# Kernel tuning notes

Measured on AMD Instinct MI355X. Metric: run time of the kernel, lower is better.

Reference implementation:

```python
import jax, jax.numpy as jnp
import numpy as np

H = 128  # hidden size
I = 256  # input size

def setup_inputs() -> dict:
    key = jax.random.key(0)
    ks = jax.random.split(key, 12)
    s_ih = 1.0 / np.sqrt(H)
    inp = {
        "x": jax.random.normal(ks[0], (256, 512, I), dtype=jnp.float32),
        # PyTorch LSTM params, gate order (i, f, g, o)
        "W_ih": jax.random.uniform(ks[1], (4 * H, I), jnp.float32, -s_ih, s_ih),
        "W_hh": jax.random.uniform(ks[2], (4 * H, H), jnp.float32, -s_ih, s_ih),
        "b_ih": jax.random.uniform(ks[3], (4 * H,), jnp.float32, -s_ih, s_ih),
        "b_hh": jax.random.uniform(ks[4], (4 * H,), jnp.float32, -s_ih, s_ih),
        "W1": jax.random.uniform(ks[5], (64, H), jnp.float32, -1/np.sqrt(H), 1/np.sqrt(H)),
        "b1": jax.random.uniform(ks[6], (64,), jnp.float32, -1/np.sqrt(H), 1/np.sqrt(H)),
        "W2": jax.random.uniform(ks[7], (32, 64), jnp.float32, -1/np.sqrt(64), 1/np.sqrt(64)),
        "b2": jax.random.uniform(ks[8], (32,), jnp.float32, -1/np.sqrt(64), 1/np.sqrt(64)),
        "W3": jax.random.uniform(ks[9], (4, 32), jnp.float32, -1/np.sqrt(32), 1/np.sqrt(32)),
        "b3": jax.random.uniform(ks[10], (4,), jnp.float32, -1/np.sqrt(32), 1/np.sqrt(32)),
    }
    return inp

def _lstm_last_hidden(x, W_ih, W_hh, b_ih, b_hh):
    B = x.shape[0]
    # Precompute input contribution for all timesteps: [B, T, 4H]
    gx = jnp.einsum("bti,gi->btg", x, W_ih) + (b_ih + b_hh)
    gx = jnp.swapaxes(gx, 0, 1)  # [T, B, 4H] for scan over time

    def step(carry, g_x):
        h, c = carry
        gates = g_x + h @ W_hh.T  # [B, 4H]
        i, f, g, o = jnp.split(gates, 4, axis=-1)
        i = jax.nn.sigmoid(i)
        f = jax.nn.sigmoid(f)
        g = jnp.tanh(g)
        o = jax.nn.sigmoid(o)
        c = f * c + i * g
        h = o * jnp.tanh(c)
        return (h, c), None

    h0 = jnp.zeros((B, H), x.dtype)
    (h, _), _ = jax.lax.scan(step, (h0, h0), gx)
    return h  # last-timestep hidden state [B, H]

def reference(x, W_ih, W_hh, b_ih, b_hh, W1, b1, W2, b2, W3, b3):
    h = _lstm_last_hidden(x, W_ih, W_hh, b_ih, b_hh)
    h = jax.nn.relu(h @ W1.T + b1)
    h = jax.nn.relu(h @ W2.T + b2)
    return h @ W3.T + b3  # [B, 4]
```

## Files before the change

### kernel.cpp

```cpp
#include <hip/hip_runtime.h>
#include <hip/hip_bf16.h>


#define TC       64
#define NCHUNK   8
#define BATCH    256
#define TSEQ     512
#define ISZ      256
#define HSZ      128
#define RB       4
#define NBLK     (BATCH / RB)
#define NGB      (2 * TC * 4)
#define HROW     144
#define GX_PER_T 131072
#define GXCH     ((size_t)TC * GX_PER_T)
#define STRT     32768
#define PF       4

#define XN       (BATCH * TSEQ * ISZ)
#define WIHN     (4 * HSZ * ISZ)
#define WHHN     (4 * HSZ * HSZ)
#define CVT_UNITS ((XN + WIHN + WHHN) / 8)

typedef __attribute__((ext_vector_type(8))) short short8;
typedef __attribute__((ext_vector_type(4))) float f32x4;

__device__ __forceinline__ void barrier_nodrain() {
    __asm__ __volatile__("s_waitcnt lgkmcnt(0)\n\ts_barrier" ::: "memory");
}

__device__ __forceinline__ float fast_rcp(float x) {
    return __builtin_amdgcn_rcpf(x);
}
__device__ __forceinline__ float sigmoidf_(float x) {
    return fast_rcp(1.0f + __expf(-x));
}
__device__ __forceinline__ float tanhf_(float x) {
    float e = __expf(2.0f * x);
    return 1.0f - 2.0f * fast_rcp(e + 1.0f);
}
__device__ __forceinline__ unsigned short f2bf(float x) {
    union { float f; unsigned u; } v; v.f = x;
    unsigned r = v.u + 0x7fffu + ((v.u >> 16) & 1u);
    return (unsigned short)(r >> 16);
}
__device__ __forceinline__ float bf2f(unsigned short b) {
    union { unsigned u; float f; } v;
    v.u = ((unsigned)b) << 16;
    return v.f;
}
__device__ __forceinline__ unsigned packbf(float lo, float hi) {
    __hip_bfloat162 h2 = __float22bfloat162_rn(make_float2(lo, hi));
    union { __hip_bfloat162 h; unsigned u; } v; v.h = h2;
    return v.u;
}
__device__ __forceinline__ float sel4(f32x4 v, int r) {
    float s01 = (r & 1) ? v[1] : v[0];
    float s23 = (r & 1) ? v[3] : v[2];
    return (r & 2) ? s23 : s01;
}

__global__ __launch_bounds__(256) void conv_kernel(
    const float* __restrict__ x, const float* __restrict__ Wih,
    const float* __restrict__ Whh,
    unsigned short* __restrict__ xb, unsigned short* __restrict__ wihb,
    unsigned short* __restrict__ whhb)
{
    const size_t stride = (size_t)gridDim.x * 256;
    for (size_t u = (size_t)blockIdx.x * 256 + threadIdx.x; u < (size_t)CVT_UNITS;
         u += stride) {
        const size_t e0 = u * 8;
        const float* s; unsigned short* d;
        if (e0 < (size_t)XN)               { s = x + e0;                 d = xb + e0; }
        else if (e0 < (size_t)(XN + WIHN)) { s = Wih + (e0 - XN);        d = wihb + (e0 - XN); }
        else                               { s = Whh + (e0 - XN - WIHN); d = whhb + (e0 - XN - WIHN); }
        float4 f0 = *(const float4*)(s);
        float4 f1 = *(const float4*)(s + 4);
        *(uint4*)(d) = (uint4){packbf(f0.x, f0.y), packbf(f0.z, f0.w),
                               packbf(f1.x, f1.y), packbf(f1.z, f1.w)};
    }
}

__global__ __launch_bounds__(512, 2) void fused_kernel(
    const unsigned short* __restrict__ xb, const unsigned short* __restrict__ wihb,
    const unsigned short* __restrict__ whhb,
    const float* __restrict__ bih, const float* __restrict__ bhh,
    const unsigned short* __restrict__ gxl, unsigned short* __restrict__ gxg,
    float* __restrict__ hc, int t0, int first, int run_lstm, int run_gemm)
{
    __shared__ __align__(16) char smem[32768];
    const int tid  = threadIdx.x;
    const int w    = tid >> 6;
    const int lane = tid & 63;
    const int n    = lane & 15;
    const int quad = lane >> 4;

    if (blockIdx.x >= NBLK) {
        if (!run_gemm) return;
        short* As = (short*)smem;
        short* Bs = (short*)(smem + 16384);

        const int gb = (int)blockIdx.x - NBLK;
        const int nt = gb & 3;
        const int mt = gb >> 2;
        const int tl = mt >> 1;
        const int b0 = (mt & 1) * 128;
        const int n0 = nt * 128;

        const int mq = w & 1;
        const int nq = w >> 1;

        const int srow = tid >> 2;
        const int skh  = (tid & 3) * 8;

        const unsigned short* xr = xb + ((size_t)(b0 + srow) * TSEQ + (size_t)(t0 + tl)) * ISZ + skh;
        const unsigned short* wr = wihb + (size_t)(n0 + srow) * ISZ + skh;

        f32x4 acc[4][2];
#pragma unroll
        for (int mi = 0; mi < 4; ++mi)
#pragma unroll
            for (int ni = 0; ni < 2; ++ni)
                acc[mi][ni] = (f32x4){0.f, 0.f, 0.f, 0.f};

        *(short8*)(&As[srow * 32 + skh]) = *(const short8*)(xr);
        *(short8*)(&Bs[srow * 32 + skh]) = *(const short8*)(wr);
        barrier_nodrain();

        for (int ks = 0; ks < 8; ++ks) {
            const int cur = (ks & 1) * 4096;
            const int nxt = 4096 - cur;
            short8 va, vb;
            if (ks < 7) {
                va = *(const short8*)(xr + (ks + 1) * 32);
                vb = *(const short8*)(wr + (ks + 1) * 32);
            }
            short8 af[4], bfr[2];
#pragma unroll
            for (int mi = 0; mi < 4; ++mi)
                af[mi] = *(const short8*)(&As[cur + (mq * 64 + mi * 16 + n) * 32 + quad * 8]);
#pragma unroll
            for (int ni = 0; ni < 2; ++ni)
                bfr[ni] = *(const short8*)(&Bs[cur + (nq * 32 + ni * 16 + n) * 32 + quad * 8]);
#pragma unroll
            for (int mi = 0; mi < 4; ++mi)
#pragma unroll
                for (int ni = 0; ni < 2; ++ni)
                    acc[mi][ni] = __builtin_amdgcn_mfma_f32_16x16x32_bf16(
                        af[mi], bfr[ni], acc[mi][ni], 0, 0, 0);
            if (ks < 7) {
                *(short8*)(&As[nxt + srow * 32 + skh]) = va;
                *(short8*)(&Bs[nxt + srow * 32 + skh]) = vb;
            }
            barrier_nodrain();
        }

#pragma unroll
        for (int ni = 0; ni < 2; ++ni) {
            const int j    = nq * 32 + ni * 16 + n;
            const int gate = n0 + j;
            const float bias = bih[gate] + bhh[gate];
            const int wj = nq * 2 + ni;
#pragma unroll
            for (int mi = 0; mi < 4; ++mi) {
                const int bb   = b0 + mq * 64 + mi * 16 + quad * 4;
                const int blk2 = bb >> 2;
                const size_t idx = ((((size_t)nt * TC + tl) * 64 + blk2) * 512) +
                                   (size_t)wj * 64 + (size_t)n * 4;
                const unsigned lo = packbf(acc[mi][ni][0] + bias, acc[mi][ni][1] + bias);
                const unsigned hi = packbf(acc[mi][ni][2] + bias, acc[mi][ni][3] + bias);
                *(uint2*)(&gxg[idx]) = (uint2){lo, hi};
            }
        }
        return;
    }

    if (!run_lstm) return;
    __builtin_amdgcn_s_setprio(1);
    short* h_lds = (short*)smem;

    const int blk  = (int)blockIdx.x;
    const int b0   = blk * RB;
    const int nb   = lane & 3;
    const int jl   = lane >> 2;
    const int j    = 16 * w + jl;
    const int rsel = jl & 3;

    short8 Af[4][4];
#pragma unroll
    for (int g = 0; g < 4; ++g) {
        const unsigned short* rowb = whhb + (size_t)(128 * g + 16 * w + n) * HSZ + 8 * quad;
#pragma unroll
        for (int ks = 0; ks < 4; ++ks)
            Af[g][ks] = *(const short8*)(rowb + 32 * ks);
    }

    float c1 = 0.f, hl1 = 0.f;
    {
        unsigned short h0 = 0;
        if (!first) {
            c1 = hc[(size_t)BATCH * HSZ + (size_t)(b0 + nb) * HSZ + j];
            h0 = f2bf(hc[(size_t)(b0 + nb) * HSZ + j]);
        }
        *(unsigned short*)&h_lds[nb * HROW + j] = h0;
    }

    const unsigned short* gp[4];
#pragma unroll
    for (int g = 0; g < 4; ++g)
        gp[g] = gxl + (((size_t)g * TC) * 64 + blk) * 512 + (size_t)w * 64 + lane;

    unsigned short gq[PF][4];
#pragma unroll
    for (int d = 0; d < PF; ++d)
#pragma unroll
        for (int g = 0; g < 4; ++g)
            gq[d][g] = gp[g][(size_t)d * STRT];

    barrier_nodrain();

    for (int t = 0; t < TC; t += PF) {
#pragma unroll
        for (int u = 0; u < PF; ++u) {
            const int tt = t + u;
            const short* hb_r = h_lds + (u & 1) * (RB * HROW);
            short*       hb_w = h_lds + ((u & 1) ^ 1) * (RB * HROW);

            short8 Bf[4];
#pragma unroll
            for (int ks = 0; ks < 4; ++ks)
                Bf[ks] = *(const short8*)(&hb_r[nb * HROW + 32 * ks + 8 * quad]);

            f32x4 acc[4];
#pragma unroll
            for (int g = 0; g < 4; ++g)
                acc[g] = __builtin_amdgcn_mfma_f32_16x16x32_bf16(
                    Af[g][0], Bf[0], (f32x4){0.f, 0.f, 0.f, 0.f}, 0, 0, 0);
#pragma unroll
            for (int ks = 1; ks < 4; ++ks)
#pragma unroll
                for (int g = 0; g < 4; ++g)
                    acc[g] = __builtin_amdgcn_mfma_f32_16x16x32_bf16(
                        Af[g][ks], Bf[ks], acc[g], 0, 0, 0);

            const float s0 = sel4(acc[0], rsel) + bf2f(gq[u][0]);
            const float s1 = sel4(acc[1], rsel) + bf2f(gq[u][1]);
            const float s2 = sel4(acc[2], rsel) + bf2f(gq[u][2]);
            const float s3 = sel4(acc[3], rsel) + bf2f(gq[u][3]);

            const int tf = (tt + PF < TC) ? (tt + PF) : (TC - 1);
#pragma unroll
            for (int g = 0; g < 4; ++g)
                gq[u][g] = gp[g][(size_t)tf * STRT];

            const float ig = sigmoidf_(s0);
            const float fg = sigmoidf_(s1);
            const float gg = tanhf_(s2);
            const float og = sigmoidf_(s3);
            c1  = fg * c1 + ig * gg;
            hl1 = og * tanhf_(c1);

            *(unsigned short*)&hb_w[nb * HROW + j] = f2bf(hl1);
            barrier_nodrain();
        }
    }

    hc[(size_t)(b0 + nb) * HSZ + j] = hl1;
    hc[(size_t)BATCH * HSZ + (size_t)(b0 + nb) * HSZ + j] = c1;
}

__global__ __launch_bounds__(64) void head_kernel(
    const float* __restrict__ hc,
    const float* __restrict__ W1, const float* __restrict__ b1,
    const float* __restrict__ W2, const float* __restrict__ b2,
    const float* __restrict__ W3, const float* __restrict__ b3,
    float* __restrict__ out)
{
    __shared__ float hs[HSZ];
    __shared__ float o1[64];
    __shared__ float o2[32];
    const int bidx = blockIdx.x;
    const int t = threadIdx.x;
    hs[t]      = hc[bidx * HSZ + t];
    hs[t + 64] = hc[bidx * HSZ + t + 64];
    __syncthreads();
    {
        float a = b1[t];
#pragma unroll 8
        for (int k = 0; k < HSZ; ++k) a += W1[t * HSZ + k] * hs[k];
        o1[t] = fmaxf(a, 0.0f);
    }
    __syncthreads();
    if (t < 32) {
        float a = b2[t];
#pragma unroll 8
        for (int k = 0; k < 64; ++k) a += W2[t * 64 + k] * o1[k];
        o2[t] = fmaxf(a, 0.0f);
    }
    __syncthreads();
    if (t < 4) {
        float a = b3[t];
#pragma unroll
        for (int k = 0; k < 32; ++k) a += W3[t * 32 + k] * o2[k];
        out[bidx * 4 + t] = a;
    }
}

extern "C" void kernel_launch(void* const* d_in, const int* in_sizes, int n_in,
                              void* d_out, int out_size, void* d_ws, size_t ws_size,
                              hipStream_t stream) {
    const float* x   = (const float*)d_in[0];
    const float* Wih = (const float*)d_in[1];
    const float* Whh = (const float*)d_in[2];
    const float* bih = (const float*)d_in[3];
    const float* bhh = (const float*)d_in[4];
    const float* W1  = (const float*)d_in[5];
    const float* b1  = (const float*)d_in[6];
    const float* W2  = (const float*)d_in[7];
    const float* b2  = (const float*)d_in[8];
    const float* W3  = (const float*)d_in[9];
    const float* b3  = (const float*)d_in[10];
    float* out = (float*)d_out;

    const size_t GXB = GXCH * sizeof(unsigned short);
    unsigned short* gx0 = (unsigned short*)d_ws;
    unsigned short* gx1 = (unsigned short*)((char*)d_ws + GXB);
    float* hc = (float*)((char*)d_ws + 2 * GXB);
    unsigned short* xb   = (unsigned short*)((char*)d_ws + 2 * GXB + 262144);
    unsigned short* wihb = xb + (size_t)XN;
    unsigned short* whhb = wihb + WIHN;

    conv_kernel<<<dim3(2048), 256, 0, stream>>>(x, Wih, Whh, xb, wihb, whhb);

    for (int k = 0; k <= NCHUNK; ++k) {
        const int run_gemm = (k < NCHUNK);
        const int run_lstm = (k > 0);
        unsigned short* gg = (k & 1) ? gx1 : gx0;
        const unsigned short* gl = ((k - 1) & 1) ? gx1 : gx0;
        fused_kernel<<<dim3(NBLK + NGB), 512, 0, stream>>>(
            xb, wihb, whhb, bih, bhh, gl, gg, hc,
            k * TC, (k == 1) ? 1 : 0, run_lstm, run_gemm);
    }

    head_kernel<<<dim3(BATCH), 64, 0, stream>>>(hc, W1, b1, W2, b2, W3, b3, out);
}
```

Measured before the change: 560.5 us.

## Interleave two batch groups per LSTM block to overlap MFMA with gate math

Each LSTM block now processes 8 batch rows as two groups of 4 whose recurrence steps are staggered. While the h·W_hh MFMAs for one group issue, the sigmoid/tanh gate math and h write for the other group run, hiding the serial latency of each timestep. This halves the number of LSTM blocks, leaving more CUs for the concurrent input-projection GEMM blocks. The occupancy hint is raised from 2 to 4 waves per EU. The added register state and extra phases per step may raise register pressure or lengthen the critical path if the overlap does not materialize.

```diff
diff --git a/kernel.cpp b/kernel.cpp
--- a/kernel.cpp
+++ b/kernel.cpp
@@ -8,14 +8,12 @@
 #define TSEQ     512
 #define ISZ      256
 #define HSZ      128
-#define RB       4
-#define NBLK     (BATCH / RB)
+#define NLB      32
 #define NGB      (2 * TC * 4)
 #define HROW     144
 #define GX_PER_T 131072
 #define GXCH     ((size_t)TC * GX_PER_T)
 #define STRT     32768
-#define PF       4
 
 #define XN       (BATCH * TSEQ * ISZ)
 #define WIHN     (4 * HSZ * ISZ)
@@ -28,7 +26,6 @@
 __device__ __forceinline__ void barrier_nodrain() {
     __asm__ __volatile__("s_waitcnt lgkmcnt(0)\n\ts_barrier" ::: "memory");
 }
-
 __device__ __forceinline__ float fast_rcp(float x) {
     return __builtin_amdgcn_rcpf(x);
 }
@@ -81,7 +78,7 @@
     }
 }
 
-__global__ __launch_bounds__(512, 2) void fused_kernel(
+__global__ __launch_bounds__(512, 4) void fused_kernel(
     const unsigned short* __restrict__ xb, const unsigned short* __restrict__ wihb,
     const unsigned short* __restrict__ whhb,
     const float* __restrict__ bih, const float* __restrict__ bhh,
@@ -95,12 +92,12 @@
     const int n    = lane & 15;
     const int quad = lane >> 4;
 
-    if (blockIdx.x >= NBLK) {
+    if (blockIdx.x >= NLB) {
         if (!run_gemm) return;
         short* As = (short*)smem;
         short* Bs = (short*)(smem + 16384);
 
-        const int gb = (int)blockIdx.x - NBLK;
+        const int gb = (int)blockIdx.x - NLB;
         const int nt = gb & 3;
         const int mt = gb >> 2;
         const int tl = mt >> 1;
@@ -177,10 +174,11 @@
 
     if (!run_lstm) return;
     __builtin_amdgcn_s_setprio(1);
-    short* h_lds = (short*)smem;
+    short* hA = (short*)smem;
+    short* hB = (short*)(smem + 4 * HROW * 2);
 
     const int blk  = (int)blockIdx.x;
-    const int b0   = blk * RB;
+    const int b0   = blk * 8;
     const int nb   = lane & 3;
     const int jl   = lane >> 2;
     const int j    = 16 * w + jl;
@@ -195,78 +193,118 @@
             Af[g][ks] = *(const short8*)(rowb + 32 * ks);
     }
 
-    float c1 = 0.f, hl1 = 0.f;
+    float cA = 0.f, cB = 0.f, hlA = 0.f, hlB = 0.f;
     {
-        unsigned short h0 = 0;
+        unsigned short h0a = 0, h0b = 0;
         if (!first) {
-            c1 = hc[(size_t)BATCH * HSZ + (size_t)(b0 + nb) * HSZ + j];
-            h0 = f2bf(hc[(size_t)(b0 + nb) * HSZ + j]);
+            cA  = hc[(size_t)BATCH * HSZ + (size_t)(b0 + nb) * HSZ + j];
+            cB  = hc[(size_t)BATCH * HSZ + (size_t)(b0 + 4 + nb) * HSZ + j];
+            h0a = f2bf(hc[(size_t)(b0 + nb) * HSZ + j]);
+            h0b = f2bf(hc[(size_t)(b0 + 4 + nb) * HSZ + j]);
         }
-        *(unsigned short*)&h_lds[nb * HROW + j] = h0;
-    }
-
-    const unsigned short* gp[4];
-#pragma unroll
-    for (int g = 0; g < 4; ++g)
-        gp[g] = gxl + (((size_t)g * TC) * 64 + blk) * 512 + (size_t)w * 64 + lane;
-
-    unsigned short gq[PF][4];
-#pragma unroll
-    for (int d = 0; d < PF; ++d)
+        *(unsigned short*)&hA[nb * HROW + j] = h0a;
+        *(unsigned short*)&hB[nb * HROW + j] = h0b;
+    }
+
+    const unsigned short* gpA[4];
+    const unsigned short* gpB[4];
+#pragma unroll
+    for (int g = 0; g < 4; ++g) {
+        gpA[g] = gxl + ((size_t)g * TC * 64 + 2 * blk) * 512 + w * 64 + lane;
+        gpB[g] = gpA[g] + 512;
+    }
+    unsigned short gqA[2][4], gqB[2][4];
+#pragma unroll
+    for (int s = 0; s < 2; ++s)
+#pragma unroll
+        for (int g = 0; g < 4; ++g) {
+            gqA[s][g] = gpA[g][(size_t)s * STRT];
+            gqB[s][g] = gpB[g][(size_t)s * STRT];
+        }
+
+    float sA0 = 0.f, sA1 = 0.f, sA2 = 0.f, sA3 = 0.f;
+    float sB0, sB1, sB2, sB3;
+
+    barrier_nodrain();
+
+    {
+        short8 Bf_[4];
+#pragma unroll
+        for (int ks = 0; ks < 4; ++ks)
+            Bf_[ks] = *(const short8*)(&hB[nb * HROW + 32 * ks + 8 * quad]);
+        f32x4 acc_[4];
 #pragma unroll
         for (int g = 0; g < 4; ++g)
-            gq[d][g] = gp[g][(size_t)d * STRT];
-
-    barrier_nodrain();
-
-    for (int t = 0; t < TC; t += PF) {
-#pragma unroll
-        for (int u = 0; u < PF; ++u) {
-            const int tt = t + u;
-            const short* hb_r = h_lds + (u & 1) * (RB * HROW);
-            short*       hb_w = h_lds + ((u & 1) ^ 1) * (RB * HROW);
-
-            short8 Bf[4];
-#pragma unroll
-            for (int ks = 0; ks < 4; ++ks)
-                Bf[ks] = *(const short8*)(&hb_r[nb * HROW + 32 * ks + 8 * quad]);
-
-            f32x4 acc[4];
+            acc_[g] = __builtin_amdgcn_mfma_f32_16x16x32_bf16(
+                Af[g][0], Bf_[0], (f32x4){0.f, 0.f, 0.f, 0.f}, 0, 0, 0);
+#pragma unroll
+        for (int ks = 1; ks < 4; ++ks)
 #pragma unroll
             for (int g = 0; g < 4; ++g)
-                acc[g] = __builtin_amdgcn_mfma_f32_16x16x32_bf16(
-                    Af[g][0], Bf[0], (f32x4){0.f, 0.f, 0.f, 0.f}, 0, 0, 0);
-#pragma unroll
-            for (int ks = 1; ks < 4; ++ks)
-#pragma unroll
-                for (int g = 0; g < 4; ++g)
-                    acc[g] = __builtin_amdgcn_mfma_f32_16x16x32_bf16(
-                        Af[g][ks], Bf[ks], acc[g], 0, 0, 0);
-
-            const float s0 = sel4(acc[0], rsel) + bf2f(gq[u][0]);
-            const float s1 = sel4(acc[1], rsel) + bf2f(gq[u][1]);
-            const float s2 = sel4(acc[2], rsel) + bf2f(gq[u][2]);
-            const float s3 = sel4(acc[3], rsel) + bf2f(gq[u][3]);
-
-            const int tf = (tt + PF < TC) ? (tt + PF) : (TC - 1);
-#pragma unroll
-            for (int g = 0; g < 4; ++g)
-                gq[u][g] = gp[g][(size_t)tf * STRT];
-
-            const float ig = sigmoidf_(s0);
-            const float fg = sigmoidf_(s1);
-            const float gg = tanhf_(s2);
-            const float og = sigmoidf_(s3);
-            c1  = fg * c1 + ig * gg;
-            hl1 = og * tanhf_(c1);
-
-            *(unsigned short*)&hb_w[nb * HROW + j] = f2bf(hl1);
-            barrier_nodrain();
-        }
-    }
-
-    hc[(size_t)(b0 + nb) * HSZ + j] = hl1;
-    hc[(size_t)BATCH * HSZ + (size_t)(b0 + nb) * HSZ + j] = c1;
+                acc_[g] = __builtin_amdgcn_mfma_f32_16x16x32_bf16(
+                    Af[g][ks], Bf_[ks], acc_[g], 0, 0, 0);
+        sB0 = sel4(acc_[0], rsel); sB1 = sel4(acc_[1], rsel);
+        sB2 = sel4(acc_[2], rsel); sB3 = sel4(acc_[3], rsel);
+    }
+
+#define PHASE(HSRC, SA0_, SA1_, SA2_, SA3_, SG0_, SG1_, SG2_, SG3_,            \
+              GQ, GP, TF, cG, hlG, HDST)                                       \
+    {                                                                          \
+        short8 Bf_[4];                                                         \
+        _Pragma("unroll")                                                      \
+        for (int ks_ = 0; ks_ < 4; ++ks_)                                      \
+            Bf_[ks_] = *(const short8*)(&HSRC[nb * HROW + 32 * ks_ + 8 * quad]);\
+        {                                                                      \
+            const float x0_ = SG0_ + bf2f(GQ[0]);                              \
+            const float x1_ = SG1_ + bf2f(GQ[1]);                              \
+            const float x2_ = SG2_ + bf2f(GQ[2]);                              \
+            const float x3_ = SG3_ + bf2f(GQ[3]);                              \
+            const float ig_ = sigmoidf_(x0_);                                  \
+            const float fg_ = sigmoidf_(x1_);                                  \
+            const float gg_ = tanhf_(x2_);                                     \
+            const float og_ = sigmoidf_(x3_);                                  \
+            cG = fg_ * cG + ig_ * gg_;                                         \
+            hlG = og_ * tanhf_(cG);                                            \
+            *(unsigned short*)&HDST[nb * HROW + j] = f2bf(hlG);                \
+        }                                                                      \
+        f32x4 acc_[4];                                                         \
+        _Pragma("unroll")                                                      \
+        for (int g_ = 0; g_ < 4; ++g_)                                         \
+            acc_[g_] = __builtin_amdgcn_mfma_f32_16x16x32_bf16(                \
+                Af[g_][0], Bf_[0], (f32x4){0.f, 0.f, 0.f, 0.f}, 0, 0, 0);      \
+        _Pragma("unroll")                                                      \
+        for (int ks_ = 1; ks_ < 4; ++ks_)                                      \
+            _Pragma("unroll")                                                  \
+            for (int g_ = 0; g_ < 4; ++g_)                                     \
+                acc_[g_] = __builtin_amdgcn_mfma_f32_16x16x32_bf16(            \
+                    Af[g_][ks_], Bf_[ks_], acc_[g_], 0, 0, 0);                 \
+        SA0_ = sel4(acc_[0], rsel); SA1_ = sel4(acc_[1], rsel);                \
+        SA2_ = sel4(acc_[2], rsel); SA3_ = sel4(acc_[3], rsel);                \
+        {                                                                      \
+            const int tc_ = (TF) < TC ? (TF) : (TC - 1);                       \
+            _Pragma("unroll")                                                  \
+            for (int g_ = 0; g_ < 4; ++g_)                                     \
+                GQ[g_] = GP[g_][(size_t)tc_ * STRT];                           \
+        }                                                                      \
+        barrier_nodrain();                                                     \
+    }
+
+    for (int t = 0; t < TC; t += 2) {
+        PHASE(hA, sA0, sA1, sA2, sA3, sB0, sB1, sB2, sB3,
+              gqB[0], gpB, t + 2, cB, hlB, hB);
+        PHASE(hB, sB0, sB1, sB2, sB3, sA0, sA1, sA2, sA3,
+              gqA[0], gpA, t + 2, cA, hlA, hA);
+        PHASE(hA, sA0, sA1, sA2, sA3, sB0, sB1, sB2, sB3,
+              gqB[1], gpB, t + 3, cB, hlB, hB);
+        PHASE(hB, sB0, sB1, sB2, sB3, sA0, sA1, sA2, sA3,
+              gqA[1], gpA, t + 3, cA, hlA, hA);
+    }
+#undef PHASE
+
+    hc[(size_t)(b0 + nb) * HSZ + j] = hlA;
+    hc[(size_t)BATCH * HSZ + (size_t)(b0 + nb) * HSZ + j] = cA;
+    hc[(size_t)(b0 + 4 + nb) * HSZ + j] = hlB;
+    hc[(size_t)BATCH * HSZ + (size_t)(b0 + 4 + nb) * HSZ + j] = cB;
 }
 
 __global__ __launch_bounds__(64) void head_kernel(
@@ -337,7 +375,7 @@
         const int run_lstm = (k > 0);
         unsigned short* gg = (k & 1) ? gx1 : gx0;
         const unsigned short* gl = ((k - 1) & 1) ? gx1 : gx0;
-        fused_kernel<<<dim3(NBLK + NGB), 512, 0, stream>>>(
+        fused_kernel<<<dim3(NLB + NGB), 512, 0, stream>>>(
             xb, wihb, whhb, bih, bhh, gl, gg, hc,
             k * TC, (k == 1) ? 1 : 0, run_lstm, run_gemm);
     }
```

Measured after the change: 1.386 ms. 147% more time.
